# Performance work log

Hardware: AMD Instinct MI355X
Metric: run time of the kernel (lower is better)

The kernel has to match this reference:

```python
import jax, jax.numpy as jnp
import numpy as np

K = 3  # number of nearest neighbors for interpolation
BIG = 1e10  # masks out cross-batch pairs in the distance matrix


def setup_inputs() -> dict:
    key = jax.random.key(0)
    ks = jax.random.split(key, 8)
    N, Ns, C, Cs, B = 4096, 16384, 256, 128, 4
    Din, H = C + Cs, 256
    return {
        "x": jax.random.normal(ks[0], (N, C), dtype=jnp.float32),
        "pos": jax.random.normal(ks[1], (N, 3), dtype=jnp.float32),
        "batch": jnp.sort(jax.random.randint(ks[2], (N,), 0, B)),
        "x_skip": jax.random.normal(ks[3], (Ns, Cs), dtype=jnp.float32),
        "pos_skip": jax.random.normal(ks[4], (Ns, 3), dtype=jnp.float32),
        "batch_skip": jnp.sort(jax.random.randint(ks[5], (Ns,), 0, B)),
        "W1": jax.random.normal(ks[6], (Din, H), dtype=jnp.float32) * (1.0 / np.sqrt(Din)),
        "b1": jnp.zeros((H,), dtype=jnp.float32),
        "W2": jax.random.normal(ks[7], (H, H), dtype=jnp.float32) * (1.0 / np.sqrt(H)),
        "b2": jnp.zeros((H,), dtype=jnp.float32),
    }


def reference(x, pos, batch, x_skip, pos_skip, batch_skip, W1, b1, W2, b2):
    # knn_interpolate: squared distances from each fine point to all coarse points,
    # masked so neighbors only come from the same batch element.
    d2 = jnp.sum((pos_skip[:, None, :] - pos[None, :, :]) ** 2, axis=-1)  # [Ns, N]
    d2 = jnp.where(batch_skip[:, None] != batch[None, :], BIG, d2)
    neg_d2, idx = jax.lax.top_k(-d2, K)          # k smallest distances, [Ns, K]
    w = 1.0 / jnp.clip(-neg_d2, 1e-16)           # inverse-squared-distance weights
    num = jnp.sum(x[idx] * w[..., None], axis=1)  # [Ns, C] weighted gather-reduce
    y = num / jnp.sum(w, axis=1, keepdims=True)
    # concat skip features, then MLP (Linear-ReLU-Linear-ReLU)
    y = jnp.concatenate([y, x_skip], axis=1)      # [Ns, C + Cs]
    h = jax.nn.relu(y @ W1 + b1)
    out = jax.nn.relu(h @ W2 + b2)
    return (out, pos_skip, batch_skip)
```

## Files before the change

### kernel.cpp

```cpp
#include <hip/hip_runtime.h>
#include <stdint.h>

#define NPTS   4096
#define NSKIP  16384
#define CCH    256
#define CSK    128
#define DIN    384
#define HDIM   256
#define BIGF   1e10f

typedef unsigned short u16;
typedef __attribute__((ext_vector_type(8))) short short8;
typedef __attribute__((ext_vector_type(4))) float floatx4;

__device__ __forceinline__ u16 f2bf(float f) {
    union { float f; uint32_t u; } c; c.f = f;
    uint32_t u = c.u;
    return (u16)((u + 0x7FFFu + ((u >> 16) & 1u)) >> 16);
}

__device__ __forceinline__ double pkkey(float d, int j) {
    return __hiloint2double(__float_as_int(d), j);
}

__global__ __launch_bounds__(256) void pack_all_kernel(
    const float* __restrict__ W1, const float* __restrict__ W2,
    u16* __restrict__ W1p, u16* __restrict__ W2p,
    const int* __restrict__ batch, int* __restrict__ range)
{
    const int bid = blockIdx.x;
    const int t = threadIdx.x;

    const float* W = (bid < 48) ? W1 : W2;
    u16* Wp       = (bid < 48) ? W1p : W2p;
    const int KT  = (bid < 48) ? 12 : 8;
    const int g   = ((bid < 48) ? bid : (bid - 48)) * 256 + t;

    const int lane = g & 63;
    const int kt = (g >> 6) % KT;
    const int nt = (g >> 6) / KT;
    const int kbase = kt * 32 + (lane >> 4) * 8;
    const int n = nt * 16 + (lane & 15);
    u16 v[8];
#pragma unroll
    for (int j = 0; j < 8; ++j) v[j] = f2bf(W[(size_t)(kbase + j) * HDIM + n]);
#pragma unroll
    for (int j = 0; j < 8; ++j) Wp[(size_t)g * 8 + j] = v[j];

    if (bid == 0) {
        for (int j = t * 16; j < t * 16 + 16; ++j) {
            if (j == 0) {
                const int b0 = batch[0];
                for (int b = 0; b <= b0; ++b) range[b] = 0;
            } else {
                const int bp = batch[j - 1], bj = batch[j];
                for (int b = bp + 1; b <= bj; ++b) range[b] = j;
            }
            if (j == NPTS - 1) {
                const int bl = batch[NPTS - 1];
                for (int b = bl + 1; b <= 4; ++b) range[b] = NPTS;
            }
        }
    }
}

__global__ __launch_bounds__(256) void knn_kernel(
    const float* __restrict__ pos, const int* __restrict__ range,
    const float* __restrict__ pos_skip, const int* __restrict__ batch_skip,
    int* __restrict__ idx3, float* __restrict__ w3)
{
    const int t = threadIdx.x;
    const int i = blockIdx.x * 16 + (t >> 4);
    const int sub = t & 15;
    const int b = batch_skip[i];
    const int start = range[b], end = range[b + 1];

    const float px = pos_skip[i * 3 + 0];
    const float py = pos_skip[i * 3 + 1];
    const float pz = pos_skip[i * 3 + 2];

    const double BIGKEY = pkkey(BIGF, 0x7FFFFFFF);
    double k0 = BIGKEY, k1 = BIGKEY, k2 = BIGKEY;

    for (int j = start + sub; j < end; j += 16) {
        const float dx = __fsub_rn(px, pos[j * 3 + 0]);
        const float dy = __fsub_rn(py, pos[j * 3 + 1]);
        const float dz = __fsub_rn(pz, pos[j * 3 + 2]);
        const float dd = __fadd_rn(__fadd_rn(__fmul_rn(dx, dx), __fmul_rn(dy, dy)),
                                   __fmul_rn(dz, dz));
        const double kk = pkkey(dd, j);
        const double u0 = fmax(k0, kk); k0 = fmin(k0, kk);
        const double u1 = fmax(k1, u0); k1 = fmin(k1, u0);
        k2 = fmin(k2, u1);
    }

#pragma unroll
    for (int m = 1; m < 16; m <<= 1) {
        const double o0 = __shfl_xor(k0, m);
        const double o1 = __shfl_xor(k1, m);
        const double o2 = __shfl_xor(k2, m);
        double u0 = fmax(k0, o0); k0 = fmin(k0, o0);
        double u1 = fmax(k1, u0); k1 = fmin(k1, u0);
        k2 = fmin(k2, u1);
        u1 = fmax(k1, o1); k1 = fmin(k1, o1);
        k2 = fmin(k2, u1);
        k2 = fmin(k2, o2);
    }

    if (sub == 0) {
        const float d0 = __int_as_float(__double2hiint(k0));
        const float d1 = __int_as_float(__double2hiint(k1));
        const float d2 = __int_as_float(__double2hiint(k2));
        const float w0 = 1.0f / fmaxf(d0, 1e-16f);
        const float w1 = 1.0f / fmaxf(d1, 1e-16f);
        const float w2 = 1.0f / fmaxf(d2, 1e-16f);
        const float inv = 1.0f / (w0 + w1 + w2);
        idx3[i * 3 + 0] = __double2loint(k0);
        idx3[i * 3 + 1] = __double2loint(k1);
        idx3[i * 3 + 2] = __double2loint(k2);
        w3[i * 3 + 0] = w0 * inv; w3[i * 3 + 1] = w1 * inv; w3[i * 3 + 2] = w2 * inv;
    }
}

__global__ __launch_bounds__(256) void fused_mlp_kernel(
    const float* __restrict__ x, const float* __restrict__ x_skip,
    const int* __restrict__ idx3, const float* __restrict__ w3,
    const u16* __restrict__ W1p, const float* __restrict__ b1,
    const u16* __restrict__ W2p, const float* __restrict__ b2,
    const float* __restrict__ pos_skip, const int* __restrict__ batch_skip,
    float* __restrict__ out)
{
    __shared__ u16 sA[32 * 392];
    const int t = threadIdx.x;
    const int row0 = blockIdx.x * 32;

#pragma unroll
    for (int k = 0; k < 8; ++k) {
        const int g = t + 256 * k;
        const int row = g >> 6, c4 = g & 63;
        const int R = row0 + row;
        const int i0 = idx3[R * 3 + 0], i1 = idx3[R * 3 + 1], i2 = idx3[R * 3 + 2];
        const float w0 = w3[R * 3 + 0], w1 = w3[R * 3 + 1], w2 = w3[R * 3 + 2];
        const float4 v0 = *(const float4*)(x + (size_t)i0 * CCH + c4 * 4);
        const float4 v1 = *(const float4*)(x + (size_t)i1 * CCH + c4 * 4);
        const float4 v2 = *(const float4*)(x + (size_t)i2 * CCH + c4 * 4);
        const float a  = w0 * v0.x + w1 * v1.x + w2 * v2.x;
        const float bq = w0 * v0.y + w1 * v1.y + w2 * v2.y;
        const float cq = w0 * v0.z + w1 * v1.z + w2 * v2.z;
        const float dq = w0 * v0.w + w1 * v1.w + w2 * v2.w;
        uint2 pk;
        pk.x = (uint32_t)f2bf(a)  | ((uint32_t)f2bf(bq) << 16);
        pk.y = (uint32_t)f2bf(cq) | ((uint32_t)f2bf(dq) << 16);
        *(uint2*)(sA + row * 392 + c4 * 4) = pk;
    }
#pragma unroll
    for (int k = 0; k < 4; ++k) {
        const int g = t + 256 * k;
        const int row = g >> 5, c4 = g & 31;
        const float4 v = *(const float4*)(x_skip + (size_t)(row0 + row) * CSK + c4 * 4);
        uint2 pk;
        pk.x = (uint32_t)f2bf(v.x) | ((uint32_t)f2bf(v.y) << 16);
        pk.y = (uint32_t)f2bf(v.z) | ((uint32_t)f2bf(v.w) << 16);
        *(uint2*)(sA + row * 392 + CCH + c4 * 4) = pk;
    }
    __syncthreads();

    const int wave = t >> 6, lane = t & 63;
    const int quad = lane >> 4, ml = lane & 15;

    floatx4 acc[2][4] = {};
    {
        const u16* aA = sA + ml * 392 + quad * 8;
        for (int kt = 0; kt < 12; ++kt) {
            short8 a0 = *(const short8*)(aA + kt * 32);
            short8 a1 = *(const short8*)(aA + 16 * 392 + kt * 32);
#pragma unroll
            for (int nt = 0; nt < 4; ++nt) {
                const int ntile = wave * 4 + nt;
                short8 bfr = *(const short8*)(W1p + (size_t)((ntile * 12 + kt) * 64 + lane) * 8);
                acc[0][nt] = __builtin_amdgcn_mfma_f32_16x16x32_bf16(a0, bfr, acc[0][nt], 0, 0, 0);
                acc[1][nt] = __builtin_amdgcn_mfma_f32_16x16x32_bf16(a1, bfr, acc[1][nt], 0, 0, 0);
            }
        }
    }
    __syncthreads();

#pragma unroll
    for (int mt = 0; mt < 2; ++mt) {
#pragma unroll
        for (int nt = 0; nt < 4; ++nt) {
            const int n = (wave * 4 + nt) * 16 + ml;
            const float bv = b1[n];
#pragma unroll
            for (int r = 0; r < 4; ++r) {
                const int m = mt * 16 + quad * 4 + r;
                sA[m * 264 + n] = f2bf(fmaxf(acc[mt][nt][r] + bv, 0.0f));
            }
        }
    }
    __syncthreads();

    floatx4 acc2[2][4] = {};
    {
        const u16* aH = sA + ml * 264 + quad * 8;
        for (int kt = 0; kt < 8; ++kt) {
            short8 a0 = *(const short8*)(aH + kt * 32);
            short8 a1 = *(const short8*)(aH + 16 * 264 + kt * 32);
#pragma unroll
            for (int nt = 0; nt < 4; ++nt) {
                const int ntile = wave * 4 + nt;
                short8 bfr = *(const short8*)(W2p + (size_t)((ntile * 8 + kt) * 64 + lane) * 8);
                acc2[0][nt] = __builtin_amdgcn_mfma_f32_16x16x32_bf16(a0, bfr, acc2[0][nt], 0, 0, 0);
                acc2[1][nt] = __builtin_amdgcn_mfma_f32_16x16x32_bf16(a1, bfr, acc2[1][nt], 0, 0, 0);
            }
        }
    }

#pragma unroll
    for (int mt = 0; mt < 2; ++mt) {
#pragma unroll
        for (int nt = 0; nt < 4; ++nt) {
            const int n = (wave * 4 + nt) * 16 + ml;
            const float bv = b2[n];
#pragma unroll
            for (int r = 0; r < 4; ++r) {
                const int m = row0 + mt * 16 + quad * 4 + r;
                out[(size_t)m * HDIM + n] = fmaxf(acc2[mt][nt][r] + bv, 0.0f);
            }
        }
    }

    if (t < 128) {
        const int e = blockIdx.x * 128 + t;
        const size_t base = (size_t)NSKIP * HDIM;
        if (e < NSKIP * 3) out[base + e] = pos_skip[e];
        else               out[base + e] = (float)batch_skip[e - NSKIP * 3];
    }
}

extern "C" void kernel_launch(void* const* d_in, const int* in_sizes, int n_in,
                              void* d_out, int out_size, void* d_ws, size_t ws_size,
                              hipStream_t stream) {
    const float* x         = (const float*)d_in[0];
    const float* pos       = (const float*)d_in[1];
    const int*   batch     = (const int*)d_in[2];
    const float* x_skip    = (const float*)d_in[3];
    const float* pos_skip  = (const float*)d_in[4];
    const int*   batch_skip= (const int*)d_in[5];
    const float* W1        = (const float*)d_in[6];
    const float* b1        = (const float*)d_in[7];
    const float* W2        = (const float*)d_in[8];
    const float* b2        = (const float*)d_in[9];
    float* out = (float*)d_out;

    char* ws = (char*)d_ws;
    int*   idx3  = (int*)ws;
    float* w3    = (float*)(ws + 196608);
    u16*   W1p   = (u16*)(ws + 393216);
    u16*   W2p   = (u16*)(ws + 589824);
    int*   range = (int*)(ws + 720896);

    pack_all_kernel<<<80, 256, 0, stream>>>(W1, W2, W1p, W2p, batch, range);
    knn_kernel<<<NSKIP / 16, 256, 0, stream>>>(pos, range, pos_skip, batch_skip, idx3, w3);
    fused_mlp_kernel<<<NSKIP / 32, 256, 0, stream>>>(x, x_skip, idx3, w3,
                                                     W1p, b1, W2p, b2,
                                                     pos_skip, batch_skip, out);
}
```

Measured before the change: 130.1 us.

## Fuse kNN search into the MLP kernel and pad positions to float4

Merges the kNN search kernel into the fused gather+MLP kernel. Each 256-thread block now first finds the 3 nearest neighbours for its 32 rows, using 8 threads per row, and keeps indices and weights in shared memory instead of a global round trip. The prep kernel also repacks coarse positions into float4 so each point is a single vector load. This removes one launch and the idx3/w3 global traffic, but the kNN phase now runs with 8 lanes per point and 512 blocks instead of 16 lanes and 1024 blocks, which may lengthen the serial distance scan.

```diff
diff --git a/kernel.cpp b/kernel.cpp
--- a/kernel.cpp
+++ b/kernel.cpp
@@ -23,9 +23,10 @@
     return __hiloint2double(__float_as_int(d), j);
 }
 
-__global__ __launch_bounds__(256) void pack_all_kernel(
+__global__ __launch_bounds__(256) void prep_kernel(
     const float* __restrict__ W1, const float* __restrict__ W2,
     u16* __restrict__ W1p, u16* __restrict__ W2p,
+    const float* __restrict__ pos, float4* __restrict__ pos4,
     const int* __restrict__ batch, int* __restrict__ range)
 {
     const int bid = blockIdx.x;
@@ -46,6 +47,11 @@
     for (int j = 0; j < 8; ++j) v[j] = f2bf(W[(size_t)(kbase + j) * HDIM + n]);
 #pragma unroll
     for (int j = 0; j < 8; ++j) Wp[(size_t)g * 8 + j] = v[j];
+
+    if (bid >= 48 && bid < 64) {
+        const int p = (bid - 48) * 256 + t;
+        pos4[p] = make_float4(pos[p * 3 + 0], pos[p * 3 + 1], pos[p * 3 + 2], 0.0f);
+    }
 
     if (bid == 0) {
         for (int j = t * 16; j < t * 16 + 16; ++j) {
@@ -64,83 +70,84 @@
     }
 }
 
-__global__ __launch_bounds__(256) void knn_kernel(
-    const float* __restrict__ pos, const int* __restrict__ range,
+__global__ __launch_bounds__(256) void mega_kernel(
+    const float* __restrict__ x, const float* __restrict__ x_skip,
+    const float4* __restrict__ pos4, const int* __restrict__ range,
     const float* __restrict__ pos_skip, const int* __restrict__ batch_skip,
-    int* __restrict__ idx3, float* __restrict__ w3)
-{
-    const int t = threadIdx.x;
-    const int i = blockIdx.x * 16 + (t >> 4);
-    const int sub = t & 15;
-    const int b = batch_skip[i];
-    const int start = range[b], end = range[b + 1];
-
-    const float px = pos_skip[i * 3 + 0];
-    const float py = pos_skip[i * 3 + 1];
-    const float pz = pos_skip[i * 3 + 2];
-
-    const double BIGKEY = pkkey(BIGF, 0x7FFFFFFF);
-    double k0 = BIGKEY, k1 = BIGKEY, k2 = BIGKEY;
-
-    for (int j = start + sub; j < end; j += 16) {
-        const float dx = __fsub_rn(px, pos[j * 3 + 0]);
-        const float dy = __fsub_rn(py, pos[j * 3 + 1]);
-        const float dz = __fsub_rn(pz, pos[j * 3 + 2]);
-        const float dd = __fadd_rn(__fadd_rn(__fmul_rn(dx, dx), __fmul_rn(dy, dy)),
-                                   __fmul_rn(dz, dz));
-        const double kk = pkkey(dd, j);
-        const double u0 = fmax(k0, kk); k0 = fmin(k0, kk);
-        const double u1 = fmax(k1, u0); k1 = fmin(k1, u0);
-        k2 = fmin(k2, u1);
-    }
-
-#pragma unroll
-    for (int m = 1; m < 16; m <<= 1) {
-        const double o0 = __shfl_xor(k0, m);
-        const double o1 = __shfl_xor(k1, m);
-        const double o2 = __shfl_xor(k2, m);
-        double u0 = fmax(k0, o0); k0 = fmin(k0, o0);
-        double u1 = fmax(k1, u0); k1 = fmin(k1, u0);
-        k2 = fmin(k2, u1);
-        u1 = fmax(k1, o1); k1 = fmin(k1, o1);
-        k2 = fmin(k2, u1);
-        k2 = fmin(k2, o2);
-    }
-
-    if (sub == 0) {
-        const float d0 = __int_as_float(__double2hiint(k0));
-        const float d1 = __int_as_float(__double2hiint(k1));
-        const float d2 = __int_as_float(__double2hiint(k2));
-        const float w0 = 1.0f / fmaxf(d0, 1e-16f);
-        const float w1 = 1.0f / fmaxf(d1, 1e-16f);
-        const float w2 = 1.0f / fmaxf(d2, 1e-16f);
-        const float inv = 1.0f / (w0 + w1 + w2);
-        idx3[i * 3 + 0] = __double2loint(k0);
-        idx3[i * 3 + 1] = __double2loint(k1);
-        idx3[i * 3 + 2] = __double2loint(k2);
-        w3[i * 3 + 0] = w0 * inv; w3[i * 3 + 1] = w1 * inv; w3[i * 3 + 2] = w2 * inv;
-    }
-}
-
-__global__ __launch_bounds__(256) void fused_mlp_kernel(
-    const float* __restrict__ x, const float* __restrict__ x_skip,
-    const int* __restrict__ idx3, const float* __restrict__ w3,
     const u16* __restrict__ W1p, const float* __restrict__ b1,
     const u16* __restrict__ W2p, const float* __restrict__ b2,
-    const float* __restrict__ pos_skip, const int* __restrict__ batch_skip,
     float* __restrict__ out)
 {
     __shared__ u16 sA[32 * 392];
+    __shared__ int   sIdx[32 * 3];
+    __shared__ float sWt[32 * 3];
     const int t = threadIdx.x;
     const int row0 = blockIdx.x * 32;
+
+    {
+        const int sub = t & 7;
+        const int lp = t >> 3;
+        const int i = row0 + lp;
+        const int b = batch_skip[i];
+        const int start = range[b], end = range[b + 1];
+
+        const float px = pos_skip[i * 3 + 0];
+        const float py = pos_skip[i * 3 + 1];
+        const float pz = pos_skip[i * 3 + 2];
+
+        const double BIGKEY = pkkey(BIGF, 0x7FFFFFFF);
+        double k0 = BIGKEY, k1 = BIGKEY, k2 = BIGKEY;
+
+        for (int j = start + sub; j < end; j += 8) {
+            const float4 q = pos4[j];
+            const float dx = __fsub_rn(px, q.x);
+            const float dy = __fsub_rn(py, q.y);
+            const float dz = __fsub_rn(pz, q.z);
+            const float dd = __fadd_rn(__fadd_rn(__fmul_rn(dx, dx), __fmul_rn(dy, dy)),
+                                       __fmul_rn(dz, dz));
+            const double kk = pkkey(dd, j);
+            const double u0 = fmax(k0, kk); k0 = fmin(k0, kk);
+            const double u1 = fmax(k1, u0); k1 = fmin(k1, u0);
+            k2 = fmin(k2, u1);
+        }
+
+#pragma unroll
+        for (int m = 1; m < 8; m <<= 1) {
+            const double o0 = __shfl_xor(k0, m);
+            const double o1 = __shfl_xor(k1, m);
+            const double o2 = __shfl_xor(k2, m);
+            double u0 = fmax(k0, o0); k0 = fmin(k0, o0);
+            double u1 = fmax(k1, u0); k1 = fmin(k1, u0);
+            k2 = fmin(k2, u1);
+            u1 = fmax(k1, o1); k1 = fmin(k1, o1);
+            k2 = fmin(k2, u1);
+            k2 = fmin(k2, o2);
+        }
+
+        if (sub == 0) {
+            const float d0 = __int_as_float(__double2hiint(k0));
+            const float d1 = __int_as_float(__double2hiint(k1));
+            const float d2 = __int_as_float(__double2hiint(k2));
+            const float w0 = 1.0f / fmaxf(d0, 1e-16f);
+            const float w1 = 1.0f / fmaxf(d1, 1e-16f);
+            const float w2 = 1.0f / fmaxf(d2, 1e-16f);
+            const float inv = 1.0f / (w0 + w1 + w2);
+            sIdx[lp * 3 + 0] = __double2loint(k0);
+            sIdx[lp * 3 + 1] = __double2loint(k1);
+            sIdx[lp * 3 + 2] = __double2loint(k2);
+            sWt[lp * 3 + 0] = w0 * inv;
+            sWt[lp * 3 + 1] = w1 * inv;
+            sWt[lp * 3 + 2] = w2 * inv;
+        }
+    }
+    __syncthreads();
 
 #pragma unroll
     for (int k = 0; k < 8; ++k) {
         const int g = t + 256 * k;
         const int row = g >> 6, c4 = g & 63;
-        const int R = row0 + row;
-        const int i0 = idx3[R * 3 + 0], i1 = idx3[R * 3 + 1], i2 = idx3[R * 3 + 2];
-        const float w0 = w3[R * 3 + 0], w1 = w3[R * 3 + 1], w2 = w3[R * 3 + 2];
+        const int i0 = sIdx[row * 3 + 0], i1 = sIdx[row * 3 + 1], i2 = sIdx[row * 3 + 2];
+        const float w0 = sWt[row * 3 + 0], w1 = sWt[row * 3 + 1], w2 = sWt[row * 3 + 2];
         const float4 v0 = *(const float4*)(x + (size_t)i0 * CCH + c4 * 4);
         const float4 v1 = *(const float4*)(x + (size_t)i1 * CCH + c4 * 4);
         const float4 v2 = *(const float4*)(x + (size_t)i2 * CCH + c4 * 4);
@@ -254,15 +261,13 @@
     float* out = (float*)d_out;
 
     char* ws = (char*)d_ws;
-    int*   idx3  = (int*)ws;
-    float* w3    = (float*)(ws + 196608);
-    u16*   W1p   = (u16*)(ws + 393216);
-    u16*   W2p   = (u16*)(ws + 589824);
-    int*   range = (int*)(ws + 720896);
-
-    pack_all_kernel<<<80, 256, 0, stream>>>(W1, W2, W1p, W2p, batch, range);
-    knn_kernel<<<NSKIP / 16, 256, 0, stream>>>(pos, range, pos_skip, batch_skip, idx3, w3);
-    fused_mlp_kernel<<<NSKIP / 32, 256, 0, stream>>>(x, x_skip, idx3, w3,
-                                                     W1p, b1, W2p, b2,
-                                                     pos_skip, batch_skip, out);
-}
+    u16*    W1p   = (u16*)ws;
+    u16*    W2p   = (u16*)(ws + 196608);
+    int*    range = (int*)(ws + 327680);
+    float4* pos4  = (float4*)(ws + 327712);
+
+    prep_kernel<<<80, 256, 0, stream>>>(W1, W2, W1p, W2p, pos, pos4, batch, range);
+    mega_kernel<<<NSKIP / 32, 256, 0, stream>>>(x, x_skip, pos4, range,
+                                                pos_skip, batch_skip,
+                                                W1p, b1, W2p, b2, out);
+}
```

Result: slower. 138.2 us (+6.2%).
